# Kernel tuning notes

Hardware: AMD Instinct MI355X
Metric: run time of the kernel (lower is better)

Reference implementation:

```python
import jax, jax.numpy as jnp
import numpy as np

N_NODES = 50000
N_EDGES = 600000
D = 128
L = 4
N_GRAPHS = 64
N_PATIENTS = 50
LAMBDA = 1.0

@jax.custom_vjp
def grl(x):
    return x

def _grl_fwd(x):
    return x, None

def _grl_bwd(_, g):
    return (-LAMBDA * g,)

grl.defvjp(_grl_fwd, _grl_bwd)


def setup_inputs() -> dict:
    key = jax.random.key(0)
    ks = jax.random.split(key, 16)
    x = jax.random.normal(ks[0], (N_NODES, D), dtype=jnp.float32)
    edge_index = jax.random.randint(ks[1], (2, N_EDGES), 0, N_NODES, dtype=jnp.int32)
    batch = jnp.sort(jax.random.randint(ks[2], (N_NODES,), 0, N_GRAPHS, dtype=jnp.int32))
    s = 1.0 / np.sqrt(D)
    W_root = jax.random.normal(ks[3], (L, D, D), dtype=jnp.float32) * s
    W_rel = jax.random.normal(ks[4], (L, D, D), dtype=jnp.float32) * s
    b_conv = jnp.zeros((L, D), dtype=jnp.float32)
    ln_gamma = jnp.ones((L, D), dtype=jnp.float32)
    ln_beta = jnp.zeros((L, D), dtype=jnp.float32)
    boundary_W = jax.random.normal(ks[5], (D, 1), dtype=jnp.float32) * s
    boundary_b = jnp.zeros((1,), dtype=jnp.float32)
    dom_W1 = jax.random.normal(ks[6], (D, D // 2), dtype=jnp.float32) * s
    dom_b1 = jnp.zeros((D // 2,), dtype=jnp.float32)
    dom_W2 = jax.random.normal(ks[7], (D // 2, N_PATIENTS), dtype=jnp.float32) * (1.0 / np.sqrt(D // 2))
    dom_b2 = jnp.zeros((N_PATIENTS,), dtype=jnp.float32)
    return {"x": x, "edge_index": edge_index, "batch": batch,
            "W_root": W_root, "W_rel": W_rel, "b_conv": b_conv,
            "ln_gamma": ln_gamma, "ln_beta": ln_beta,
            "boundary_W": boundary_W, "boundary_b": boundary_b,
            "dom_W1": dom_W1, "dom_b1": dom_b1,
            "dom_W2": dom_W2, "dom_b2": dom_b2}


def _layernorm(h, gamma, beta, eps=1e-5):
    mu = jnp.mean(h, axis=-1, keepdims=True)
    var = jnp.var(h, axis=-1, keepdims=True)
    return (h - mu) * jax.lax.rsqrt(var + eps) * gamma + beta


def reference(x, edge_index, batch, W_root, W_rel, b_conv, ln_gamma, ln_beta,
              boundary_W, boundary_b, dom_W1, dom_b1, dom_W2, dom_b2):
    src, dst = edge_index[0], edge_index[1]
    n = x.shape[0]
    for l in range(L):
        x_in = x
        msg = x[src] @ W_rel[l]                                   # [E, D] gather + GEMM
        agg = jax.ops.segment_sum(msg, dst, num_segments=n)        # [N, D] scatter-add
        h = x @ W_root[l] + agg + b_conv[l]
        h = _layernorm(h, ln_gamma[l], ln_beta[l])
        h = jax.nn.elu(h)
        # dropout p=model.dropout in eval mode -> identity
        x = h + x_in                                               # residual (shapes match)
    boundary_logits = (x @ boundary_W + boundary_b)[:, 0]          # [N]
    pooled = jax.ops.segment_sum(x, batch, num_segments=N_GRAPHS)  # [G, D]
    counts = jax.ops.segment_sum(jnp.ones((n, 1), x.dtype), batch, num_segments=N_GRAPHS)
    pooled = pooled / jnp.clip(counts, 1.0)
    r = grl(pooled)                                                # GRL: identity fwd
    h = jax.nn.elu(r @ dom_W1 + dom_b1)                            # Dropout(0.1) eval -> identity
    domain_logits = h @ dom_W2 + dom_b2                            # [G, n_patients]
    return boundary_logits, domain_logits
```

## Files before the change

### kernel.cpp

```cpp
#include <hip/hip_runtime.h>
#include <cstdint>
#include <cstddef>

#define N_NODES   50000
#define N_EDGES   600000
#define DIM       128
#define NLAYERS   4
#define N_GRAPHS  64
#define N_PATIENTS 50
#define ROWS      32

typedef __attribute__((ext_vector_type(8))) __bf16        bf16x8;
typedef __attribute__((ext_vector_type(4))) float         f32x4;
typedef __attribute__((ext_vector_type(4))) unsigned int  u32x4;
typedef __attribute__((ext_vector_type(8))) unsigned short u16x8;

__device__ inline unsigned short f2bf(float f) {
    unsigned u = __builtin_bit_cast(unsigned, f);
    u += 0x7FFFu + ((u >> 16) & 1u);
    return (unsigned short)(u >> 16);
}

__device__ inline float bf2f(unsigned short s) {
    return __builtin_bit_cast(float, (unsigned)s << 16);
}

__device__ inline f32x4 lo4(u16x8 u) {
    f32x4 r;
    r[0] = bf2f(u[0]); r[1] = bf2f(u[1]); r[2] = bf2f(u[2]); r[3] = bf2f(u[3]);
    return r;
}
__device__ inline f32x4 hi4(u16x8 u) {
    f32x4 r;
    r[0] = bf2f(u[4]); r[1] = bf2f(u[5]); r[2] = bf2f(u[6]); r[3] = bf2f(u[7]);
    return r;
}


__global__ void k_count(const int* __restrict__ ei, int* __restrict__ counts) {
    int e = blockIdx.x * 256 + threadIdx.x;
    if (e < N_EDGES) atomicAdd(&counts[ei[N_EDGES + e]], 1);
}

__global__ void k_scan_a(const int* __restrict__ counts, int* __restrict__ incl,
                         int* __restrict__ bsums, int n) {
    __shared__ int s[256];
    int i = blockIdx.x * 256 + threadIdx.x;
    int v = (i < n) ? counts[i] : 0;
    s[threadIdx.x] = v;
    __syncthreads();
    for (int off = 1; off < 256; off <<= 1) {
        int t = (threadIdx.x >= off) ? s[threadIdx.x - off] : 0;
        __syncthreads();
        s[threadIdx.x] += t;
        __syncthreads();
    }
    if (i < n) incl[i] = s[threadIdx.x];
    if (threadIdx.x == 255) bsums[blockIdx.x] = s[255];
}

__global__ void k_scan_b(int* __restrict__ bsums, int nb) {
    __shared__ int s[256];
    int t = threadIdx.x;
    int v = (t < nb) ? bsums[t] : 0;
    s[t] = v;
    __syncthreads();
    for (int off = 1; off < 256; off <<= 1) {
        int u = (t >= off) ? s[t - off] : 0;
        __syncthreads();
        s[t] += u;
        __syncthreads();
    }
    if (t < nb) bsums[t] = s[t];
}

__global__ void k_scan_c(const int* __restrict__ counts, const int* __restrict__ incl,
                         const int* __restrict__ bsums, int* __restrict__ row_ptr,
                         int* __restrict__ cursor, int n) {
    int i = blockIdx.x * 256 + threadIdx.x;
    if (i < n) {
        int off = blockIdx.x ? bsums[blockIdx.x - 1] : 0;
        int ex  = incl[i] - counts[i] + off;
        row_ptr[i] = ex;
        cursor[i]  = ex;
        if (i == n - 1) row_ptr[n] = incl[i] + off;
    }
}

__global__ void k_fill(const int* __restrict__ ei, int* __restrict__ cursor,
                       int* __restrict__ esorted) {
    int e = blockIdx.x * 256 + threadIdx.x;
    if (e < N_EDGES) {
        int d   = ei[N_EDGES + e];
        int pos = atomicAdd(&cursor[d], 1);
        esorted[pos] = ei[e];
    }
}


__global__ void k_prep(const float* __restrict__ x, unsigned short* __restrict__ xb) {
    int idx = blockIdx.x * 256 + threadIdx.x;
    if (idx < N_NODES * DIM / 8) {
        f32x4 v0 = *(const f32x4*)(x + (size_t)idx * 8);
        f32x4 v1 = *(const f32x4*)(x + (size_t)idx * 8 + 4);
        u16x8 o = { f2bf(v0[0]), f2bf(v0[1]), f2bf(v0[2]), f2bf(v0[3]),
                    f2bf(v1[0]), f2bf(v1[1]), f2bf(v1[2]), f2bf(v1[3]) };
        *(u16x8*)(xb + (size_t)idx * 8) = o;
    }
}


__global__ void k_wt(const float* __restrict__ Wroot, const float* __restrict__ Wrel,
                     unsigned short* __restrict__ Wt) {
    int idx = blockIdx.x * 256 + threadIdx.x;
    if (idx < NLAYERS * DIM * 256) {
        int l = idx >> 15;
        int c = (idx >> 8) & 127;
        int k = idx & 255;
        float v = (k < 128) ? Wroot[l * 16384 + k * 128 + c]
                            : Wrel[l * 16384 + (k - 128) * 128 + c];
        Wt[idx] = f2bf(v);
    }
}


__global__ __launch_bounds__(512, 8) void k_layer(
    const unsigned short* __restrict__ xb,
    unsigned short* __restrict__ xbnext,
    const int* __restrict__ row_ptr, const int* __restrict__ esrc,
    const unsigned short* __restrict__ Wt,
    const float* __restrict__ bconv, const float* __restrict__ gamma,
    const float* __restrict__ beta,
    const float* __restrict__ bW, const float* __restrict__ bb,
    float* __restrict__ boundary, int last)
{
    __shared__ __align__(16) unsigned short x2s[ROWS * 256];
    __shared__ float rsum[ROWS][4], rsq[ROWS][4], rbl[ROWS][4];
    const int tid     = threadIdx.x;
    const int rowbase = blockIdx.x * ROWS;

    const int grp = tid >> 4;
    const int li  = tid & 15;

    {
        int grow = rowbase + grp;
        int rx = (grp & 7) << 4;
        u16x8 v = { 0, 0, 0, 0, 0, 0, 0, 0 };
        if (grow < N_NODES) v = *(const u16x8*)(xb + (size_t)grow * DIM + li * 8);
        int byteoff = (grp * 512 + li * 16) ^ rx;
        *(u16x8*)((char*)x2s + byteoff) = v;
    }

    {
        int grow = rowbase + grp;
        f32x4 a0 = 0.f, a1 = 0.f, b0 = 0.f, b1 = 0.f;
        int beg = 0, end = 0;
        if (grow < N_NODES) { beg = row_ptr[grow]; end = row_ptr[grow + 1]; }
        int e = beg;
        for (; e + 5 < end; e += 6) {
            int s0 = esrc[e],     s1 = esrc[e + 1], s2 = esrc[e + 2];
            int s3 = esrc[e + 3], s4 = esrc[e + 4], s5 = esrc[e + 5];
            u16x8 u0 = *(const u16x8*)(xb + (size_t)s0 * DIM + li * 8);
            u16x8 u1 = *(const u16x8*)(xb + (size_t)s1 * DIM + li * 8);
            u16x8 u2 = *(const u16x8*)(xb + (size_t)s2 * DIM + li * 8);
            u16x8 u3 = *(const u16x8*)(xb + (size_t)s3 * DIM + li * 8);
            u16x8 u4 = *(const u16x8*)(xb + (size_t)s4 * DIM + li * 8);
            u16x8 u5 = *(const u16x8*)(xb + (size_t)s5 * DIM + li * 8);
            a0 += lo4(u0); a1 += hi4(u0);
            b0 += lo4(u1); b1 += hi4(u1);
            a0 += lo4(u2); a1 += hi4(u2);
            b0 += lo4(u3); b1 += hi4(u3);
            a0 += lo4(u4); a1 += hi4(u4);
            b0 += lo4(u5); b1 += hi4(u5);
        }
        for (; e < end; ++e) {
            int s0 = esrc[e];
            u16x8 u0 = *(const u16x8*)(xb + (size_t)s0 * DIM + li * 8);
            a0 += lo4(u0); a1 += hi4(u0);
        }
        a0 += b0; a1 += b1;
        u16x8 o = { f2bf(a0[0]), f2bf(a0[1]), f2bf(a0[2]), f2bf(a0[3]),
                    f2bf(a1[0]), f2bf(a1[1]), f2bf(a1[2]), f2bf(a1[3]) };
        int byteoff = (grp * 512 + 256 + li * 16) ^ ((grp & 7) << 4);
        *(u16x8*)((char*)x2s + byteoff) = o;
    }
    __syncthreads();

    int lane = tid & 63, w = tid >> 6;
    int colb = lane & 15, kg = lane >> 4;
    int rt = w >> 2, cq = w & 3;

    u32x4 araw[8];
    {
        int row  = rt * 16 + colb;
        int base = row * 512 + kg * 16;
        int rx   = (row & 7) << 4;
        #pragma unroll
        for (int ks = 0; ks < 8; ks++) {
            int byteoff = (base + ks * 64) ^ rx;
            araw[ks] = *(const u32x4*)((const char*)x2s + byteoff);
        }
    }

    f32x4 acc[2];
    acc[0] = 0.0f; acc[1] = 0.0f;

    #pragma unroll
    for (int cb = 0; cb < 2; cb++) {
        const unsigned short* wp = Wt + ((cq * 32 + cb * 16 + colb) * 256 + kg * 8);
        #pragma unroll
        for (int ks = 0; ks < 8; ks++) {
            u32x4 braw = *(const u32x4*)(wp + ks * 32);
            acc[cb] = __builtin_amdgcn_mfma_f32_16x16x32_bf16(
                __builtin_bit_cast(bf16x8, araw[ks]),
                __builtin_bit_cast(bf16x8, braw), acc[cb], 0, 0, 0);
        }
    }

    float hv[4][2];
    #pragma unroll
    for (int j = 0; j < 4; j++) {
        float ps = 0.f, pq = 0.f;
        #pragma unroll
        for (int cb = 0; cb < 2; cb++) {
            int col = cq * 32 + cb * 16 + colb;
            float h = acc[cb][j] + bconv[col];
            hv[j][cb] = h; ps += h; pq += h * h;
        }
        #pragma unroll
        for (int m = 1; m < 16; m <<= 1) {
            ps += __shfl_xor(ps, m);
            pq += __shfl_xor(pq, m);
        }
        if (colb == 0) {
            int lr = rt * 16 + kg * 4 + j;
            rsum[lr][cq] = ps;
            rsq[lr][cq]  = pq;
        }
    }
    __syncthreads();

    #pragma unroll
    for (int j = 0; j < 4; j++) {
        int lr   = rt * 16 + kg * 4 + j;
        int grow = rowbase + lr;
        float sum = rsum[lr][0] + rsum[lr][1] + rsum[lr][2] + rsum[lr][3];
        float sq  = rsq[lr][0] + rsq[lr][1] + rsq[lr][2] + rsq[lr][3];
        float mean = sum * (1.f / 128.f);
        float var  = sq * (1.f / 128.f) - mean * mean;
        float rs   = rsqrtf(var + 1e-5f);
        float bl = 0.f;
        if (grow < N_NODES) {
            int rx = (lr & 7) << 4;
            #pragma unroll
            for (int cb = 0; cb < 2; cb++) {
                int col  = cq * 32 + cb * 16 + colb;
                float hn = (hv[j][cb] - mean) * rs * gamma[col] + beta[col];
                hn = hn > 0.f ? hn : (expf(hn) - 1.f);
                int xoff = (lr * 512 + col * 2) ^ rx;
                float xi = bf2f(*(const unsigned short*)((const char*)x2s + xoff));
                float xo = hn + xi;
                xbnext[(size_t)grow * DIM + col] = f2bf(xo);
                bl += xo * bW[col];
            }
        }
        if (last) {
            #pragma unroll
            for (int m = 1; m < 16; m <<= 1) bl += __shfl_xor(bl, m);
            if (colb == 0) rbl[lr][cq] = bl;
        }
    }
    if (last) {
        __syncthreads();
        if (tid < ROWS && rowbase + tid < N_NODES)
            boundary[rowbase + tid] = rbl[tid][0] + rbl[tid][1] + rbl[tid][2] + rbl[tid][3] + bb[0];
    }
}


__global__ void k_pool(const unsigned short* __restrict__ xb, const int* __restrict__ batch,
                       float* __restrict__ pooled, int* __restrict__ gcount) {
    __shared__ float2 s[64][4];
    int g = blockIdx.x >> 4, q = blockIdx.x & 15;
    int lo = 0, hi = N_NODES;
    while (lo < hi) { int m = (lo + hi) >> 1; if (batch[m] < g) lo = m + 1; else hi = m; }
    int s0 = lo;
    lo = 0; hi = N_NODES;
    while (lo < hi) { int m = (lo + hi) >> 1; if (batch[m] < g + 1) lo = m + 1; else hi = m; }
    int e0  = lo;
    int len = e0 - s0;
    int r0 = s0 + (int)((long long)len * q / 16);
    int r1 = s0 + (int)((long long)len * (q + 1) / 16);
    int cp = threadIdx.x & 63, rp = threadIdx.x >> 6;
    float ax = 0.f, ay = 0.f;
    for (int r = r0 + rp; r < r1; r += 4) {
        unsigned u = *(const unsigned*)(xb + (size_t)r * DIM + cp * 2);
        ax += bf2f((unsigned short)(u & 0xFFFF));
        ay += bf2f((unsigned short)(u >> 16));
    }
    s[cp][rp] = make_float2(ax, ay);
    __syncthreads();
    if (rp == 0) {
        float2 v1 = s[cp][1], v2 = s[cp][2], v3 = s[cp][3];
        ax += v1.x + v2.x + v3.x;
        ay += v1.y + v2.y + v3.y;
        atomicAdd(&pooled[g * DIM + cp * 2], ax);
        atomicAdd(&pooled[g * DIM + cp * 2 + 1], ay);
    }
    if (q == 0 && threadIdx.x == 0) gcount[g] = len;
}


__global__ __launch_bounds__(256) void k_dom1(
    const float* __restrict__ pooled, const int* __restrict__ gcount,
    const float* __restrict__ W1, const float* __restrict__ b1,
    float* __restrict__ h1g)
{
    int o = blockIdx.x * 256 + threadIdx.x;
    if (o < 64 * 64) {
        int i = o >> 6, j = o & 63;
        float cnt = (float)gcount[i];
        float rc = 1.f / (cnt < 1.f ? 1.f : cnt);
        float s = b1[j];
        #pragma unroll 8
        for (int k = 0; k < 128; k++) s += pooled[i * 128 + k] * rc * W1[k * 64 + j];
        h1g[o] = s > 0.f ? s : (expf(s) - 1.f);
    }
}

__global__ __launch_bounds__(256) void k_dom2(
    const float* __restrict__ h1g,
    const float* __restrict__ W2, const float* __restrict__ b2,
    float* __restrict__ out)
{
    int o = blockIdx.x * 256 + threadIdx.x;
    if (o < 64 * N_PATIENTS) {
        int i = o / N_PATIENTS, p = o - i * N_PATIENTS;
        float s = b2[p];
        #pragma unroll 8
        for (int k = 0; k < 64; k++) s += h1g[i * 64 + k] * W2[k * N_PATIENTS + p];
        out[o] = s;
    }
}


extern "C" void kernel_launch(void* const* d_in, const int* in_sizes, int n_in,
                              void* d_out, int out_size, void* d_ws, size_t ws_size,
                              hipStream_t stream) {
    const float* x     = (const float*)d_in[0];
    const int*   ei    = (const int*)d_in[1];
    const int*   batch = (const int*)d_in[2];
    const float* Wroot = (const float*)d_in[3];
    const float* Wrel  = (const float*)d_in[4];
    const float* bconv = (const float*)d_in[5];
    const float* gamma = (const float*)d_in[6];
    const float* beta  = (const float*)d_in[7];
    const float* bW    = (const float*)d_in[8];
    const float* bb    = (const float*)d_in[9];
    const float* W1    = (const float*)d_in[10];
    const float* b1    = (const float*)d_in[11];
    const float* W2    = (const float*)d_in[12];
    const float* b2    = (const float*)d_in[13];
    float* out = (float*)d_out;

    char* ws = (char*)d_ws;
    size_t off = 0;
    auto alloc = [&](size_t bytes) -> char* {
        char* p = ws + off;
        off += (bytes + 255) & ~(size_t)255;
        return p;
    };
    unsigned short* xbA     = (unsigned short*)alloc((size_t)N_NODES * DIM * 2);
    unsigned short* xbB     = (unsigned short*)alloc((size_t)N_NODES * DIM * 2);
    unsigned short* Wt      = (unsigned short*)alloc((size_t)NLAYERS * DIM * 256 * 2);
    int*            counts  = (int*)alloc((size_t)N_NODES * 4);
    int*            incl    = (int*)alloc((size_t)N_NODES * 4);
    int*            row_ptr = (int*)alloc((size_t)(N_NODES + 1) * 4);
    int*            cursor  = (int*)alloc((size_t)N_NODES * 4);
    int*            esorted = (int*)alloc((size_t)N_EDGES * 4);
    int*            bsums   = (int*)alloc(256 * 4);
    float*          pooled  = (float*)alloc((size_t)N_GRAPHS * DIM * 4);
    int*            gcount  = (int*)alloc((size_t)N_GRAPHS * 4);
    float*          h1g     = (float*)alloc((size_t)64 * 64 * 4);
    (void)ws_size; (void)in_sizes; (void)n_in; (void)out_size;

    hipMemsetAsync(counts, 0, (size_t)N_NODES * 4, stream);
    hipMemsetAsync(pooled, 0, (size_t)N_GRAPHS * DIM * 4, stream);

    k_wt<<<(NLAYERS * DIM * 256 + 255) / 256, 256, 0, stream>>>(Wroot, Wrel, Wt);
    k_prep<<<(N_NODES * DIM / 8 + 255) / 256, 256, 0, stream>>>(x, xbA);
    k_count<<<(N_EDGES + 255) / 256, 256, 0, stream>>>(ei, counts);
    int nb = (N_NODES + 255) / 256;
    k_scan_a<<<nb, 256, 0, stream>>>(counts, incl, bsums, N_NODES);
    k_scan_b<<<1, 256, 0, stream>>>(bsums, nb);
    k_scan_c<<<nb, 256, 0, stream>>>(counts, incl, bsums, row_ptr, cursor, N_NODES);
    k_fill<<<(N_EDGES + 255) / 256, 256, 0, stream>>>(ei, cursor, esorted);

    int lgrid = (N_NODES + ROWS - 1) / ROWS;
    const unsigned short* xbi = xbA;
    unsigned short* xbo = xbB;
    for (int l = 0; l < NLAYERS; l++) {
        int last = (l == NLAYERS - 1);
        k_layer<<<lgrid, 512, 0, stream>>>(xbi, xbo,
                                           row_ptr, esorted, Wt + (size_t)l * DIM * 256,
                                           bconv + l * DIM, gamma + l * DIM, beta + l * DIM,
                                           bW, bb, out, last);
        const unsigned short* t = xbi; xbi = xbo; xbo = (unsigned short*)t;
    }
    k_pool<<<N_GRAPHS * 16, 256, 0, stream>>>(xbi, batch, pooled, gcount);
    k_dom1<<<16, 256, 0, stream>>>(pooled, gcount, W1, b1, h1g);
    k_dom2<<<(64 * N_PATIENTS + 255) / 256, 256, 0, stream>>>(h1g, W2, b2, out + N_NODES);
}
```

Measured before the change: 315.2 us.

## Split neighbor aggregation across a wavefront with edge-parallel lanes and index prefetch

```diff
diff --git a/kernel.cpp b/kernel.cpp
--- a/kernel.cpp
+++ b/kernel.cpp
@@ -138,11 +138,10 @@
     __shared__ float rsum[ROWS][4], rsq[ROWS][4], rbl[ROWS][4];
     const int tid     = threadIdx.x;
     const int rowbase = blockIdx.x * ROWS;
-
-    const int grp = tid >> 4;
-    const int li  = tid & 15;
+    const int lane = tid & 63, w = tid >> 6;
 
     {
+        int grp = tid >> 4, li = tid & 15;
         int grow = rowbase + grp;
         int rx = (grp & 7) << 4;
         u16x8 v = { 0, 0, 0, 0, 0, 0, 0, 0 };
@@ -152,41 +151,68 @@
     }
 
     {
-        int grow = rowbase + grp;
-        f32x4 a0 = 0.f, a1 = 0.f, b0 = 0.f, b1 = 0.f;
-        int beg = 0, end = 0;
-        if (grow < N_NODES) { beg = row_ptr[grow]; end = row_ptr[grow + 1]; }
-        int e = beg;
-        for (; e + 5 < end; e += 6) {
-            int s0 = esrc[e],     s1 = esrc[e + 1], s2 = esrc[e + 2];
-            int s3 = esrc[e + 3], s4 = esrc[e + 4], s5 = esrc[e + 5];
-            u16x8 u0 = *(const u16x8*)(xb + (size_t)s0 * DIM + li * 8);
-            u16x8 u1 = *(const u16x8*)(xb + (size_t)s1 * DIM + li * 8);
-            u16x8 u2 = *(const u16x8*)(xb + (size_t)s2 * DIM + li * 8);
-            u16x8 u3 = *(const u16x8*)(xb + (size_t)s3 * DIM + li * 8);
-            u16x8 u4 = *(const u16x8*)(xb + (size_t)s4 * DIM + li * 8);
-            u16x8 u5 = *(const u16x8*)(xb + (size_t)s5 * DIM + li * 8);
-            a0 += lo4(u0); a1 += hi4(u0);
-            b0 += lo4(u1); b1 += hi4(u1);
-            a0 += lo4(u2); a1 += hi4(u2);
-            b0 += lo4(u3); b1 += hi4(u3);
-            a0 += lo4(u4); a1 += hi4(u4);
-            b0 += lo4(u5); b1 += hi4(u5);
-        }
-        for (; e < end; ++e) {
-            int s0 = esrc[e];
-            u16x8 u0 = *(const u16x8*)(xb + (size_t)s0 * DIM + li * 8);
-            a0 += lo4(u0); a1 += hi4(u0);
-        }
-        a0 += b0; a1 += b1;
-        u16x8 o = { f2bf(a0[0]), f2bf(a0[1]), f2bf(a0[2]), f2bf(a0[3]),
-                    f2bf(a1[0]), f2bf(a1[1]), f2bf(a1[2]), f2bf(a1[3]) };
-        int byteoff = (grp * 512 + 256 + li * 16) ^ ((grp & 7) << 4);
-        *(u16x8*)((char*)x2s + byteoff) = o;
+        int eo = lane >> 4, li = lane & 15;
+        int rbase = w * 4;
+        int bg[4], dg[4];
+        #pragma unroll
+        for (int r = 0; r < 4; r++) {
+            int grow = rowbase + rbase + r;
+            int b = 0, n = 0;
+            if (grow < N_NODES) { b = row_ptr[grow]; n = row_ptr[grow + 1] - b; }
+            bg[r] = b; dg[r] = n;
+        }
+        const u16x8 z = { 0, 0, 0, 0, 0, 0, 0, 0 };
+        int i0, i1, i2, i3;
+        {
+            int b = bg[0], n = dg[0];
+            i0 = (eo      < n) ? esrc[b + eo]      : -1;
+            i1 = (eo + 4  < n) ? esrc[b + eo + 4]  : -1;
+            i2 = (eo + 8  < n) ? esrc[b + eo + 8]  : -1;
+            i3 = (eo + 12 < n) ? esrc[b + eo + 12] : -1;
+        }
+        #pragma unroll
+        for (int r = 0; r < 4; r++) {
+            int n0 = -1, n1 = -1, n2 = -1, n3 = -1;
+            if (r < 3) {
+                int b = bg[r + 1], n = dg[r + 1];
+                n0 = (eo      < n) ? esrc[b + eo]      : -1;
+                n1 = (eo + 4  < n) ? esrc[b + eo + 4]  : -1;
+                n2 = (eo + 8  < n) ? esrc[b + eo + 8]  : -1;
+                n3 = (eo + 12 < n) ? esrc[b + eo + 12] : -1;
+            }
+            u16x8 v0 = z, v1 = z, v2 = z, v3 = z;
+            if (i0 >= 0) v0 = *(const u16x8*)(xb + (size_t)i0 * DIM + li * 8);
+            if (i1 >= 0) v1 = *(const u16x8*)(xb + (size_t)i1 * DIM + li * 8);
+            if (i2 >= 0) v2 = *(const u16x8*)(xb + (size_t)i2 * DIM + li * 8);
+            if (i3 >= 0) v3 = *(const u16x8*)(xb + (size_t)i3 * DIM + li * 8);
+            f32x4 a0 = (lo4(v0) + lo4(v1)) + (lo4(v2) + lo4(v3));
+            f32x4 a1 = (hi4(v0) + hi4(v1)) + (hi4(v2) + hi4(v3));
+            int n = dg[r], b = bg[r];
+            for (int e = 16; e < n; e += 4) {
+                int idx = (e + eo < n) ? esrc[b + e + eo] : -1;
+                u16x8 v = z;
+                if (idx >= 0) v = *(const u16x8*)(xb + (size_t)idx * DIM + li * 8);
+                a0 += lo4(v); a1 += hi4(v);
+            }
+            #pragma unroll
+            for (int k = 0; k < 4; k++) {
+                a0[k] += __shfl_xor(a0[k], 16);
+                a0[k] += __shfl_xor(a0[k], 32);
+                a1[k] += __shfl_xor(a1[k], 16);
+                a1[k] += __shfl_xor(a1[k], 32);
+            }
+            if (eo == 0) {
+                int row = rbase + r;
+                u16x8 o = { f2bf(a0[0]), f2bf(a0[1]), f2bf(a0[2]), f2bf(a0[3]),
+                            f2bf(a1[0]), f2bf(a1[1]), f2bf(a1[2]), f2bf(a1[3]) };
+                int byteoff = (row * 512 + 256 + li * 16) ^ ((row & 7) << 4);
+                *(u16x8*)((char*)x2s + byteoff) = o;
+            }
+            i0 = n0; i1 = n1; i2 = n2; i3 = n3;
+        }
     }
     __syncthreads();
 
-    int lane = tid & 63, w = tid >> 6;
     int colb = lane & 15, kg = lane >> 4;
     int rt = w >> 2, cq = w & 3;
 
```

Result: slower. 322.3 us (+2.3%).

## Split fused layer into aggregation and GEMM kernels, keep fp32 residual stream

Applied to the files above, without the earlier changes.

```diff
diff --git a/kernel.cpp b/kernel.cpp
--- a/kernel.cpp
+++ b/kernel.cpp
@@ -124,10 +124,52 @@
 }
 
 
-__global__ __launch_bounds__(512, 8) void k_layer(
+__global__ __launch_bounds__(256) void k_agg(
     const unsigned short* __restrict__ xb,
+    unsigned short* __restrict__ aggb,
+    const int* __restrict__ row_ptr, const int* __restrict__ esrc)
+{
+    int tid = threadIdx.x;
+    int grp = tid >> 4, li = tid & 15;
+    int grow = blockIdx.x * 16 + grp;
+    if (grow >= N_NODES) return;
+    int beg = row_ptr[grow], end = row_ptr[grow + 1];
+    f32x4 a0 = 0.f, a1 = 0.f, b0 = 0.f, b1 = 0.f;
+    int e = beg;
+    for (; e + 5 < end; e += 6) {
+        int s0 = esrc[e],     s1 = esrc[e + 1], s2 = esrc[e + 2];
+        int s3 = esrc[e + 3], s4 = esrc[e + 4], s5 = esrc[e + 5];
+        u16x8 u0 = *(const u16x8*)(xb + (size_t)s0 * DIM + li * 8);
+        u16x8 u1 = *(const u16x8*)(xb + (size_t)s1 * DIM + li * 8);
+        u16x8 u2 = *(const u16x8*)(xb + (size_t)s2 * DIM + li * 8);
+        u16x8 u3 = *(const u16x8*)(xb + (size_t)s3 * DIM + li * 8);
+        u16x8 u4 = *(const u16x8*)(xb + (size_t)s4 * DIM + li * 8);
+        u16x8 u5 = *(const u16x8*)(xb + (size_t)s5 * DIM + li * 8);
+        a0 += lo4(u0); a1 += hi4(u0);
+        b0 += lo4(u1); b1 += hi4(u1);
+        a0 += lo4(u2); a1 += hi4(u2);
+        b0 += lo4(u3); b1 += hi4(u3);
+        a0 += lo4(u4); a1 += hi4(u4);
+        b0 += lo4(u5); b1 += hi4(u5);
+    }
+    for (; e < end; ++e) {
+        int s0 = esrc[e];
+        u16x8 u0 = *(const u16x8*)(xb + (size_t)s0 * DIM + li * 8);
+        a0 += lo4(u0); a1 += hi4(u0);
+    }
+    a0 += b0; a1 += b1;
+    u16x8 o = { f2bf(a0[0]), f2bf(a0[1]), f2bf(a0[2]), f2bf(a0[3]),
+                f2bf(a1[0]), f2bf(a1[1]), f2bf(a1[2]), f2bf(a1[3]) };
+    *(u16x8*)(aggb + (size_t)grow * DIM + li * 8) = o;
+}
+
+
+__global__ __launch_bounds__(512, 4) void k_gemm(
+    const float* __restrict__ xin,
+    const unsigned short* __restrict__ xb,
+    const unsigned short* __restrict__ aggb,
+    float* __restrict__ xout,
     unsigned short* __restrict__ xbnext,
-    const int* __restrict__ row_ptr, const int* __restrict__ esrc,
     const unsigned short* __restrict__ Wt,
     const float* __restrict__ bconv, const float* __restrict__ gamma,
     const float* __restrict__ beta,
@@ -138,55 +180,23 @@
     __shared__ float rsum[ROWS][4], rsq[ROWS][4], rbl[ROWS][4];
     const int tid     = threadIdx.x;
     const int rowbase = blockIdx.x * ROWS;
-
-    const int grp = tid >> 4;
-    const int li  = tid & 15;
+    const int lane = tid & 63, w = tid >> 6;
 
     {
+        int grp = tid >> 4, li = tid & 15;
         int grow = rowbase + grp;
         int rx = (grp & 7) << 4;
         u16x8 v = { 0, 0, 0, 0, 0, 0, 0, 0 };
-        if (grow < N_NODES) v = *(const u16x8*)(xb + (size_t)grow * DIM + li * 8);
-        int byteoff = (grp * 512 + li * 16) ^ rx;
-        *(u16x8*)((char*)x2s + byteoff) = v;
-    }
-
-    {
-        int grow = rowbase + grp;
-        f32x4 a0 = 0.f, a1 = 0.f, b0 = 0.f, b1 = 0.f;
-        int beg = 0, end = 0;
-        if (grow < N_NODES) { beg = row_ptr[grow]; end = row_ptr[grow + 1]; }
-        int e = beg;
-        for (; e + 5 < end; e += 6) {
-            int s0 = esrc[e],     s1 = esrc[e + 1], s2 = esrc[e + 2];
-            int s3 = esrc[e + 3], s4 = esrc[e + 4], s5 = esrc[e + 5];
-            u16x8 u0 = *(const u16x8*)(xb + (size_t)s0 * DIM + li * 8);
-            u16x8 u1 = *(const u16x8*)(xb + (size_t)s1 * DIM + li * 8);
-            u16x8 u2 = *(const u16x8*)(xb + (size_t)s2 * DIM + li * 8);
-            u16x8 u3 = *(const u16x8*)(xb + (size_t)s3 * DIM + li * 8);
-            u16x8 u4 = *(const u16x8*)(xb + (size_t)s4 * DIM + li * 8);
-            u16x8 u5 = *(const u16x8*)(xb + (size_t)s5 * DIM + li * 8);
-            a0 += lo4(u0); a1 += hi4(u0);
-            b0 += lo4(u1); b1 += hi4(u1);
-            a0 += lo4(u2); a1 += hi4(u2);
-            b0 += lo4(u3); b1 += hi4(u3);
-            a0 += lo4(u4); a1 += hi4(u4);
-            b0 += lo4(u5); b1 += hi4(u5);
-        }
-        for (; e < end; ++e) {
-            int s0 = esrc[e];
-            u16x8 u0 = *(const u16x8*)(xb + (size_t)s0 * DIM + li * 8);
-            a0 += lo4(u0); a1 += hi4(u0);
-        }
-        a0 += b0; a1 += b1;
-        u16x8 o = { f2bf(a0[0]), f2bf(a0[1]), f2bf(a0[2]), f2bf(a0[3]),
-                    f2bf(a1[0]), f2bf(a1[1]), f2bf(a1[2]), f2bf(a1[3]) };
-        int byteoff = (grp * 512 + 256 + li * 16) ^ ((grp & 7) << 4);
-        *(u16x8*)((char*)x2s + byteoff) = o;
+        u16x8 a = { 0, 0, 0, 0, 0, 0, 0, 0 };
+        if (grow < N_NODES) {
+            v = *(const u16x8*)(xb + (size_t)grow * DIM + li * 8);
+            a = *(const u16x8*)(aggb + (size_t)grow * DIM + li * 8);
+        }
+        *(u16x8*)((char*)x2s + ((grp * 512 + li * 16) ^ rx)) = v;
+        *(u16x8*)((char*)x2s + ((grp * 512 + 256 + li * 16) ^ rx)) = a;
     }
     __syncthreads();
 
-    int lane = tid & 63, w = tid >> 6;
     int colb = lane & 15, kg = lane >> 4;
     int rt = w >> 2, cq = w & 3;
 
@@ -251,16 +261,14 @@
         float rs   = rsqrtf(var + 1e-5f);
         float bl = 0.f;
         if (grow < N_NODES) {
-            int rx = (lr & 7) << 4;
             #pragma unroll
             for (int cb = 0; cb < 2; cb++) {
                 int col  = cq * 32 + cb * 16 + colb;
                 float hn = (hv[j][cb] - mean) * rs * gamma[col] + beta[col];
                 hn = hn > 0.f ? hn : (expf(hn) - 1.f);
-                int xoff = (lr * 512 + col * 2) ^ rx;
-                float xi = bf2f(*(const unsigned short*)((const char*)x2s + xoff));
-                float xo = hn + xi;
-                xbnext[(size_t)grow * DIM + col] = f2bf(xo);
+                float xo = hn + xin[(size_t)grow * DIM + col];
+                xout[(size_t)grow * DIM + col] = xo;
+                if (xbnext) xbnext[(size_t)grow * DIM + col] = f2bf(xo);
                 bl += xo * bW[col];
             }
         }
@@ -278,9 +286,9 @@
 }
 
 
-__global__ void k_pool(const unsigned short* __restrict__ xb, const int* __restrict__ batch,
+__global__ void k_pool(const float* __restrict__ x, const int* __restrict__ batch,
                        float* __restrict__ pooled, int* __restrict__ gcount) {
-    __shared__ float2 s[64][4];
+    __shared__ float s[128];
     int g = blockIdx.x >> 4, q = blockIdx.x & 15;
     int lo = 0, hi = N_NODES;
     while (lo < hi) { int m = (lo + hi) >> 1; if (batch[m] < g) lo = m + 1; else hi = m; }
@@ -291,21 +299,14 @@
     int len = e0 - s0;
     int r0 = s0 + (int)((long long)len * q / 16);
     int r1 = s0 + (int)((long long)len * (q + 1) / 16);
-    int cp = threadIdx.x & 63, rp = threadIdx.x >> 6;
-    float ax = 0.f, ay = 0.f;
-    for (int r = r0 + rp; r < r1; r += 4) {
-        unsigned u = *(const unsigned*)(xb + (size_t)r * DIM + cp * 2);
-        ax += bf2f((unsigned short)(u & 0xFFFF));
-        ay += bf2f((unsigned short)(u >> 16));
-    }
-    s[cp][rp] = make_float2(ax, ay);
+    int col = threadIdx.x & 127, half = threadIdx.x >> 7;
+    float acc = 0.f;
+    for (int r = r0 + half; r < r1; r += 2) acc += x[(size_t)r * DIM + col];
+    if (half) s[col] = acc;
     __syncthreads();
-    if (rp == 0) {
-        float2 v1 = s[cp][1], v2 = s[cp][2], v3 = s[cp][3];
-        ax += v1.x + v2.x + v3.x;
-        ay += v1.y + v2.y + v3.y;
-        atomicAdd(&pooled[g * DIM + cp * 2], ax);
-        atomicAdd(&pooled[g * DIM + cp * 2 + 1], ay);
+    if (!half) {
+        acc += s[col];
+        atomicAdd(&pooled[g * DIM + col], acc);
     }
     if (q == 0 && threadIdx.x == 0) gcount[g] = len;
 }
@@ -370,8 +371,11 @@
         off += (bytes + 255) & ~(size_t)255;
         return p;
     };
+    float*          xA      = (float*)alloc((size_t)N_NODES * DIM * 4);
+    float*          xB      = (float*)alloc((size_t)N_NODES * DIM * 4);
     unsigned short* xbA     = (unsigned short*)alloc((size_t)N_NODES * DIM * 2);
     unsigned short* xbB     = (unsigned short*)alloc((size_t)N_NODES * DIM * 2);
+    unsigned short* aggb    = (unsigned short*)alloc((size_t)N_NODES * DIM * 2);
     unsigned short* Wt      = (unsigned short*)alloc((size_t)NLAYERS * DIM * 256 * 2);
     int*            counts  = (int*)alloc((size_t)N_NODES * 4);
     int*            incl    = (int*)alloc((size_t)N_NODES * 4);
@@ -396,18 +400,24 @@
     k_scan_c<<<nb, 256, 0, stream>>>(counts, incl, bsums, row_ptr, cursor, N_NODES);
     k_fill<<<(N_EDGES + 255) / 256, 256, 0, stream>>>(ei, cursor, esorted);
 
-    int lgrid = (N_NODES + ROWS - 1) / ROWS;
+    int agrid = (N_NODES + 15) / 16;
+    int ggrid = (N_NODES + ROWS - 1) / ROWS;
+    const float* xi = x;
+    float* xo = xA;
     const unsigned short* xbi = xbA;
     unsigned short* xbo = xbB;
     for (int l = 0; l < NLAYERS; l++) {
         int last = (l == NLAYERS - 1);
-        k_layer<<<lgrid, 512, 0, stream>>>(xbi, xbo,
-                                           row_ptr, esorted, Wt + (size_t)l * DIM * 256,
-                                           bconv + l * DIM, gamma + l * DIM, beta + l * DIM,
-                                           bW, bb, out, last);
+        k_agg<<<agrid, 256, 0, stream>>>(xbi, aggb, row_ptr, esorted);
+        k_gemm<<<ggrid, 512, 0, stream>>>(xi, xbi, aggb, xo, last ? nullptr : xbo,
+                                          Wt + (size_t)l * DIM * 256,
+                                          bconv + l * DIM, gamma + l * DIM, beta + l * DIM,
+                                          bW, bb, out, last);
+        xi = xo;
+        xo = (xo == xA) ? xB : xA;
         const unsigned short* t = xbi; xbi = xbo; xbo = (unsigned short*)t;
     }
-    k_pool<<<N_GRAPHS * 16, 256, 0, stream>>>(xbi, batch, pooled, gcount);
+    k_pool<<<N_GRAPHS * 16, 256, 0, stream>>>(xi, batch, pooled, gcount);
     k_dom1<<<16, 256, 0, stream>>>(pooled, gcount, W1, b1, h1g);
     k_dom2<<<(64 * N_PATIENTS + 255) / 256, 256, 0, stream>>>(h1g, W2, b2, out + N_NODES);
 }
```

Result: slower. 370.9 us (+17.7%).
